# Optimization experiments

Measured on AMD Instinct MI355X. Metric: run time of the kernel, lower is better.

The kernel has to match this reference:

```python
import jax, jax.numpy as jnp
import numpy as np

NUM_HEADS = 8
NUM_GROUPS = 32
EPS = 1e-5


def setup_inputs() -> dict:
    key = jax.random.key(0)
    ks = jax.random.split(key, 3)
    B, C, T = 4, 512, 2048
    x = jax.random.normal(ks[0], (B, C, T), dtype=jnp.float32)
    gn_gamma = jnp.ones((C,), jnp.float32)
    gn_beta = jnp.zeros((C,), jnp.float32)
    w_qkv = jax.random.normal(ks[1], (3 * C, C), jnp.float32) * (1.0 / np.sqrt(C))
    b_qkv = jnp.zeros((3 * C,), jnp.float32)
    w_proj = jax.random.normal(ks[2], (C, C), jnp.float32) * (1.0 / np.sqrt(C))
    b_proj = jnp.zeros((C,), jnp.float32)
    return {"x": x, "gn_gamma": gn_gamma, "gn_beta": gn_beta,
            "w_qkv": w_qkv, "b_qkv": b_qkv, "w_proj": w_proj, "b_proj": b_proj}


def _group_norm(x, gamma, beta):
    # x: [B, C, T]
    B, C, T = x.shape
    xg = x.reshape(B, NUM_GROUPS, (C // NUM_GROUPS) * T)
    mean = xg.mean(axis=-1, keepdims=True)
    var = xg.var(axis=-1, keepdims=True)
    xn = ((xg - mean) * jax.lax.rsqrt(var + EPS)).reshape(B, C, T)
    return xn * gamma[None, :, None] + beta[None, :, None]


def reference(x, gn_gamma, gn_beta, w_qkv, b_qkv, w_proj, b_proj):
    B, C, T = x.shape
    H = NUM_HEADS
    dh = C // H  # attn_ch
    scale = 1.0 / np.sqrt(np.sqrt(dh))

    h = _group_norm(x, gn_gamma, gn_beta)
    # 1x1 conv1d == channel matmul: [B, 3C, T]
    qkv = jnp.einsum('oc,bct->bot', w_qkv, h) + b_qkv[None, :, None]
    # tokens-major: [B, T, H, 3*dh]
    qkv = qkv.transpose(0, 2, 1).reshape(B, T, H, 3 * dh)
    q, k, v = jnp.split(qkv, 3, axis=-1)  # each [B, T, H, dh]

    weight = jnp.einsum('bthc,bshc->bhts', q * scale, k * scale)
    weight = jax.nn.softmax(weight.astype(jnp.float32), axis=-1).astype(qkv.dtype)
    out = jnp.einsum('bhts,bshc->bthc', weight, v).reshape(B, T, C)

    out = out.transpose(0, 2, 1)  # [B, C, T]
    y = jnp.einsum('oc,bct->bot', w_proj, out) + b_proj[None, :, None]
    return x + y
```

## Files before the change

### kernel.cpp

```cpp
#include <hip/hip_runtime.h>
#include <hip/hip_bf16.h>
#include <math.h>
#include <stdint.h>

#define Bb 4
#define Cc 512
#define Tt 2048
#define Hh 8

typedef __attribute__((ext_vector_type(8))) short short8;
typedef __attribute__((ext_vector_type(4))) float f32x4;
typedef __attribute__((ext_vector_type(8))) unsigned short u16x8;

__device__ __forceinline__ unsigned short f2bf(float f) {
  __hip_bfloat16 h = __float2bfloat16(f);
  unsigned short u;
  __builtin_memcpy(&u, &h, 2);
  return u;
}
__device__ __forceinline__ float bf2f(unsigned short u) {
  union { uint32_t i; float f; } v;
  v.i = (uint32_t)u << 16;
  return v.f;
}

__device__ __forceinline__ void async16(const void* g, void* l) {
  __builtin_amdgcn_global_load_lds(
      (const __attribute__((address_space(1))) uint32_t*)g,
      (__attribute__((address_space(3))) uint32_t*)l, 16, 0, 0);
}

__global__ __launch_bounds__(256) void gn_part(const float* __restrict__ x,
                                               float* __restrict__ part) {
  const int blk = blockIdx.x;
  const size_t base = (size_t)blk * 4096;
  const int tid = threadIdx.x;
  float s = 0.f, ss = 0.f;
#pragma unroll
  for (int k = 0; k < 4; ++k) {
    const float4 v = *(const float4*)(x + base + (size_t)(k * 256 + tid) * 4);
    s += v.x + v.y + v.z + v.w;
    ss += v.x * v.x + v.y * v.y + v.z * v.z + v.w * v.w;
  }
#pragma unroll
  for (int off = 32; off >= 1; off >>= 1) {
    s += __shfl_down(s, off);
    ss += __shfl_down(ss, off);
  }
  __shared__ float rs[4], rss[4];
  const int wid = tid >> 6;
  if ((tid & 63) == 0) { rs[wid] = s; rss[wid] = ss; }
  __syncthreads();
  if (tid == 0) {
    part[blk * 2] = rs[0] + rs[1] + rs[2] + rs[3];
    part[blk * 2 + 1] = rss[0] + rss[1] + rss[2] + rss[3];
  }
}

__global__ __launch_bounds__(128) void gn_fin(const float* __restrict__ part,
                                              float* __restrict__ stats) {
  const int g = threadIdx.x;
  float s = 0.f, ss = 0.f;
#pragma unroll
  for (int c = 0; c < 8; ++c) {
    s += part[(g * 8 + c) * 2];
    ss += part[(g * 8 + c) * 2 + 1];
  }
  const float mean = s / 32768.f;
  const float var = ss / 32768.f - mean * mean;
  stats[g * 2] = mean;
  stats[g * 2 + 1] = rsqrtf(var + 1e-5f);
}

__global__ __launch_bounds__(256) void norm_trans(const float* __restrict__ x,
                                                  const float* __restrict__ stats,
                                                  const float* __restrict__ gamma,
                                                  const float* __restrict__ beta,
                                                  unsigned short* __restrict__ hT) {
  __shared__ unsigned short Tl[64][72];
  const int tid = threadIdx.x;
  const int b = blockIdx.z, c0 = blockIdx.y * 64, t0 = blockIdx.x * 64;
  const int cl = tid >> 2, j16 = (tid & 3) * 16;
  const int c = c0 + cl;
  const int grp = c >> 4;
  const float mean = stats[((size_t)b * 32 + grp) * 2];
  const float rstd = stats[((size_t)b * 32 + grp) * 2 + 1];
  const float ga = gamma[c] * rstd;
  const float be = beta[c] - mean * ga;
  const float* src = x + ((size_t)b * Cc + c) * Tt + t0 + j16;
#pragma unroll
  for (int q = 0; q < 4; ++q) {
    const float4 v = *(const float4*)(src + q * 4);
    Tl[j16 + q * 4 + 0][cl] = f2bf(v.x * ga + be);
    Tl[j16 + q * 4 + 1][cl] = f2bf(v.y * ga + be);
    Tl[j16 + q * 4 + 2][cl] = f2bf(v.z * ga + be);
    Tl[j16 + q * 4 + 3][cl] = f2bf(v.w * ga + be);
  }
  __syncthreads();
  const int tl = tid >> 2, i16 = (tid & 3) * 16;
  unsigned short* dst = hT + ((size_t)b * Tt + t0 + tl) * Cc + c0 + i16;
  *(u16x8*)dst = *(const u16x8*)&Tl[tl][i16];
  *(u16x8*)(dst + 8) = *(const u16x8*)&Tl[tl][i16 + 8];
}

__global__ __launch_bounds__(256) void cvt_bf16_2(const float* __restrict__ a,
                                                  unsigned short* __restrict__ oa, int n4a,
                                                  const float* __restrict__ bsrc,
                                                  unsigned short* __restrict__ ob, int n4b) {
  const int i = blockIdx.x * 256 + threadIdx.x;
  const float* in;
  unsigned short* out;
  int idx;
  if (i < n4a) {
    in = a; out = oa; idx = i;
  } else if (i < n4a + n4b) {
    in = bsrc; out = ob; idx = i - n4a;
  } else {
    return;
  }
  const float4 v = *(const float4*)(in + (size_t)idx * 4);
  ushort4 o;
  o.x = f2bf(v.x); o.y = f2bf(v.y); o.z = f2bf(v.z); o.w = f2bf(v.w);
  *(ushort4*)(out + (size_t)idx * 4) = o;
}

template <int MODE, int BM>
__global__ __launch_bounds__(256) void gemm_mfma(const unsigned short* __restrict__ A,
                                                 const unsigned short* __restrict__ Bt,
                                                 const float* __restrict__ bias,
                                                 const float* __restrict__ res,
                                                 unsigned short* __restrict__ outb,
                                                 float* __restrict__ outf,
                                                 unsigned short* __restrict__ qkt,
                                                 int M) {
  constexpr int NA = BM / 32;
  __shared__ unsigned short SMEM[(BM + 128) * 64];
  unsigned short* Al = SMEM;
  unsigned short* Bl = SMEM + BM * 64;
  const int tid = threadIdx.x;
  const int n0 = blockIdx.x * 128, m0 = blockIdx.y * BM;
  const size_t z = blockIdx.z;
  const int l = tid & 63, il = l & 15, g = l >> 4;
  const int w = tid >> 6;
  const int wm = (w >> 1) * (BM / 2), wn = (w & 1) * 64;

  const unsigned short* Bz = Bt + z * (size_t)Tt * Cc;
  const unsigned short* Ap = A + (size_t)(m0 + (tid >> 2)) * Cc + (tid & 3) * 8;
  const unsigned short* Bp = Bz + (size_t)(n0 + (tid >> 2)) * Cc + (tid & 3) * 8;
  char* ldsA = (char*)Al + w * 1024;
  char* ldsB = (char*)Bl + w * 1024;

  f32x4 acc[NA][4] = {};
  for (int k0 = 0; k0 < Cc; k0 += 64) {
#pragma unroll
    for (int ks = 0; ks < 2; ++ks) {
      const int ko = k0 + ks * 32;
      async16(Ap + ko, ldsA + ks * (BM * 64));
      if (BM == 128) async16(Ap + (size_t)64 * Cc + ko, ldsA + ks * (BM * 64) + 4096);
      async16(Bp + ko, ldsB + ks * (128 * 64));
      async16(Bp + (size_t)64 * Cc + ko, ldsB + ks * (128 * 64) + 4096);
    }
    __syncthreads();
    __builtin_amdgcn_s_setprio(1);
#pragma unroll
    for (int ks = 0; ks < 2; ++ks) {
      short8 af[NA], bf[4];
#pragma unroll
      for (int i = 0; i < NA; ++i)
        af[i] = *(const short8*)(Al + ks * (BM * 32) + (wm + i * 16 + il) * 32 + g * 8);
#pragma unroll
      for (int j = 0; j < 4; ++j)
        bf[j] = *(const short8*)(Bl + ks * (128 * 32) + (wn + j * 16 + il) * 32 + g * 8);
#pragma unroll
      for (int i = 0; i < NA; ++i)
#pragma unroll
        for (int j = 0; j < 4; ++j)
          acc[i][j] = __builtin_amdgcn_mfma_f32_16x16x32_bf16(af[i], bf[j], acc[i][j], 0, 0, 0);
    }
    __builtin_amdgcn_s_setprio(0);
    __syncthreads();
  }

  if (MODE == 1) {
#pragma unroll
    for (int i = 0; i < NA; ++i) {
#pragma unroll
      for (int r = 0; r < 4; ++r) {
        const int m = m0 + wm + i * 16 + 4 * g + r;
        const float bv = bias[m];
#pragma unroll
        for (int j = 0; j < 4; ++j) {
          const int n = n0 + wn + j * 16 + il;
          const size_t idx = (z * (size_t)M + m) * Tt + n;
          outf[idx] = acc[i][j][r] + bv + res[idx];
        }
      }
    }
  } else {
    const int r0 = m0 + wm;
    const int sec = (r0 % 192) >> 6;
    const int hh = r0 / 192;
    if (sec == 2) {
#pragma unroll
      for (int i = 0; i < 4; ++i) {
#pragma unroll
        for (int r = 0; r < 4; ++r) {
          const int m = r0 + i * 16 + 4 * g + r;
          const float bv = bias[m];
#pragma unroll
          for (int j = 0; j < 4; ++j) {
            const int n = n0 + wn + j * 16 + il;
            outb[(z * (size_t)M + m) * Tt + n] = f2bf(acc[i][j][r] + bv);
          }
        }
      }
    } else {
      unsigned short (*Sc)[32][72] = (unsigned short(*)[32][72])SMEM;
      const float qs = (sec == 0) ? 0.125f * 1.44269504f : 1.0f;
      const size_t obase = ((size_t)(z * (Hh * 2)) + hh * 2 + sec) * Tt;
#pragma unroll
      for (int hf = 0; hf < 2; ++hf) {
#pragma unroll
        for (int i = 0; i < 4; ++i) {
          const int mloc = i * 16 + 4 * g;
          const float b0 = bias[r0 + mloc + 0];
          const float b1 = bias[r0 + mloc + 1];
          const float b2 = bias[r0 + mloc + 2];
          const float b3 = bias[r0 + mloc + 3];
#pragma unroll
          for (int j2 = 0; j2 < 2; ++j2) {
            const int j = hf * 2 + j2;
            ushort4 pkk;
            pkk.x = f2bf((acc[i][j][0] + b0) * qs);
            pkk.y = f2bf((acc[i][j][1] + b1) * qs);
            pkk.z = f2bf((acc[i][j][2] + b2) * qs);
            pkk.w = f2bf((acc[i][j][3] + b3) * qs);
            *(ushort4*)&Sc[w][j2 * 16 + il][mloc] = pkk;
          }
        }
        asm volatile("s_waitcnt lgkmcnt(0)" ::: "memory");
#pragma unroll
        for (int it = 0; it < 4; ++it) {
          const int row = it * 8 + (l >> 3);
          const int mcol = (l & 7) * 8;
          const u16x8 vv = *(const u16x8*)&Sc[w][row][mcol];
          const int tg = n0 + wn + hf * 32 + row;
          *(u16x8*)(qkt + (obase + tg) * 64 + mcol) = vv;
        }
        asm volatile("s_waitcnt lgkmcnt(0)" ::: "memory");
      }
    }
  }
}

__global__ __launch_bounds__(256, 4) void attn_mfma5(const unsigned short* __restrict__ qkt,
                                                     const unsigned short* __restrict__ qkvc,
                                                     unsigned short* __restrict__ attnoT) {
  __shared__ unsigned short KVs[2][2][64 * 64];

  const int tid = threadIdx.x;
  const int w = tid >> 6, l = tid & 63, il = l & 15, g = l >> 4;

  const int bid = blockIdx.x;
  const int swz = (bid & 7) * 128 + (bid >> 3);
  const int bh = swz >> 5, qt = swz & 31;
  const int b = bh >> 3, h = bh & 7;
  const int q0 = qt * 64;

  const unsigned short* Qb = qkt + (size_t)(bh * 2) * Tt * 64;
  const char* Kb = (const char*)(Qb + (size_t)Tt * 64);
  const char* Vb = (const char*)(qkvc + ((size_t)b * (3 * Cc) + h * 192 + 128) * Tt);

  short8 qf[2];
  {
    const unsigned short* qp = Qb + (size_t)(q0 + w * 16 + il) * 64 + g * 8;
    qf[0] = *(const short8*)qp;
    qf[1] = *(const short8*)(qp + 32);
  }

  union { uint32_t u[4]; short8 v; } ones;
  ones.u[0] = ones.u[1] = ones.u[2] = ones.u[3] = 0x3F803F80u;

  float m_run = 0.f;
  f32x4 acco[4] = {};
  f32x4 acc_l = {};
  uint32_t frP[2][4];

  const int srow = w * 16 + (l >> 3);
  const int scol = ((l & 7) ^ (l >> 3)) << 4;

  auto stage = [&](int buf, int s0) {
    char* kd = (char*)&KVs[buf][0][0] + w * 2048;
    char* vd = (char*)&KVs[buf][1][0] + w * 2048;
    async16(Kb + (size_t)(s0 + srow) * 128 + scol, kd);
    async16(Kb + (size_t)(s0 + srow + 8) * 128 + scol, kd + 1024);
    async16(Vb + (size_t)srow * (Tt * 2) + (size_t)s0 * 2 + scol, vd);
    async16(Vb + (size_t)(srow + 8) * (Tt * 2) + (size_t)s0 * 2 + scol, vd + 1024);
  };

  f32x4 accs[4];
  auto qk_phase = [&](int buf) {
    const float nm = -m_run;
#pragma unroll
    for (int i = 0; i < 4; ++i) {
      accs[i][0] = nm; accs[i][1] = nm; accs[i][2] = nm; accs[i][3] = nm;
    }
    const unsigned short* Kc = &KVs[buf][0][0];
#pragma unroll
    for (int ks = 0; ks < 2; ++ks) {
#pragma unroll
      for (int i = 0; i < 4; ++i) {
        const short8 kf =
            *(const short8*)(Kc + (i * 16 + il) * 64 + ((((ks << 2) + g) ^ (il & 7)) << 3));
        accs[i] = __builtin_amdgcn_mfma_f32_16x16x32_bf16(kf, qf[ks], accs[i], 0, 0, 0);
      }
    }
  };

  auto pv_phase = [&](int buf) {
    const unsigned short* Vc = &KVs[buf][1][0];
#pragma unroll
    for (int ks = 0; ks < 2; ++ks) {
      union { uint32_t u[4]; short8 v; } fu;
      fu.u[0] = frP[ks][0]; fu.u[1] = frP[ks][1];
      fu.u[2] = frP[ks][2]; fu.u[3] = frP[ks][3];
#pragma unroll
      for (int j = 0; j < 4; ++j) {
        const short8 vf =
            *(const short8*)(Vc + (j * 16 + il) * 64 + ((((ks << 2) + g) ^ (il & 7)) << 3));
        acco[j] = __builtin_amdgcn_mfma_f32_16x16x32_bf16(fu.v, vf, acco[j], 0, 0, 0);
      }
      acc_l = __builtin_amdgcn_mfma_f32_16x16x32_bf16(fu.v, ones.v, acc_l, 0, 0, 0);
    }
  };

  auto softmax_pack = [&]() {
    float pmax = fmaxf(fmaxf(fmaxf(accs[0][0], accs[0][1]), accs[0][2]), accs[0][3]);
    pmax = fmaxf(pmax, fmaxf(fmaxf(accs[1][0], accs[1][1]), fmaxf(accs[1][2], accs[1][3])));
    pmax = fmaxf(pmax, fmaxf(fmaxf(accs[2][0], accs[2][1]), fmaxf(accs[2][2], accs[2][3])));
    pmax = fmaxf(pmax, fmaxf(fmaxf(accs[3][0], accs[3][1]), fmaxf(accs[3][2], accs[3][3])));

    uint32_t pk[4][2];
    if (!__all(pmax <= 8.0f)) {
      float mx = pmax;
#pragma unroll
      for (int off = 1; off < 64; off <<= 1) mx = fmaxf(mx, __shfl_xor(mx, off));
      const float alpha = __builtin_amdgcn_exp2f(-mx);
      m_run += mx;
#pragma unroll
      for (int j = 0; j < 4; ++j) acco[j] = acco[j] * alpha;
      acc_l = acc_l * alpha;
#pragma unroll
      for (int i = 0; i < 4; ++i) {
        const float p0 = __builtin_amdgcn_exp2f(accs[i][0] - mx);
        const float p1 = __builtin_amdgcn_exp2f(accs[i][1] - mx);
        const float p2 = __builtin_amdgcn_exp2f(accs[i][2] - mx);
        const float p3 = __builtin_amdgcn_exp2f(accs[i][3] - mx);
        asm("v_cvt_pk_bf16_f32 %0, %1, %2" : "=v"(pk[i][0]) : "v"(p0), "v"(p1));
        asm("v_cvt_pk_bf16_f32 %0, %1, %2" : "=v"(pk[i][1]) : "v"(p2), "v"(p3));
      }
    } else {
#pragma unroll
      for (int i = 0; i < 4; ++i) {
        const float p0 = __builtin_amdgcn_exp2f(accs[i][0]);
        const float p1 = __builtin_amdgcn_exp2f(accs[i][1]);
        const float p2 = __builtin_amdgcn_exp2f(accs[i][2]);
        const float p3 = __builtin_amdgcn_exp2f(accs[i][3]);
        asm("v_cvt_pk_bf16_f32 %0, %1, %2" : "=v"(pk[i][0]) : "v"(p0), "v"(p1));
        asm("v_cvt_pk_bf16_f32 %0, %1, %2" : "=v"(pk[i][1]) : "v"(p2), "v"(p3));
      }
    }
#pragma unroll
    for (int ks = 0; ks < 2; ++ks) {
#pragma unroll
      for (int hh = 0; hh < 2; ++hh) {
        uint32_t a = pk[2 * ks][hh], bq = pk[2 * ks + 1][hh];
        asm("v_permlane32_swap_b32 %0, %1" : "+v"(a), "+v"(bq));
        asm("v_permlane16_swap_b32 %0, %1" : "+v"(a), "+v"(bq));
        frP[ks][hh] = a;
        frP[ks][2 + hh] = bq;
      }
    }
  };

  stage(0, 0);
  __syncthreads();
  stage(1, 64);
  __builtin_amdgcn_s_setprio(1);
  qk_phase(0);
  __builtin_amdgcn_s_setprio(0);
  softmax_pack();

  const int NT = Tt / 64;
  for (int t = 1; t < NT; ++t) {
    const int cb = t & 1, pb = cb ^ 1;
    __syncthreads();
    __builtin_amdgcn_s_setprio(1);
    qk_phase(cb);
    pv_phase(pb);
    __builtin_amdgcn_s_setprio(0);
    __syncthreads();
    if (t + 1 < NT) stage(pb, (t + 1) * 64);
    softmax_pack();
  }
  __builtin_amdgcn_s_setprio(1);
  pv_phase(1);
  __builtin_amdgcn_s_setprio(0);

#pragma unroll
  for (int r = 0; r < 4; ++r) {
    const float li = 1.f / acc_l[r];
    const int tq = q0 + w * 16 + 4 * g + r;
    unsigned short* d0 = attnoT + ((size_t)b * Tt + tq) * Cc + h * 64 + il;
#pragma unroll
    for (int j = 0; j < 4; ++j) d0[j * 16] = f2bf(acco[j][r] * li);
  }
}

extern "C" void kernel_launch(void* const* d_in, const int* in_sizes, int n_in,
                              void* d_out, int out_size, void* d_ws, size_t ws_size,
                              hipStream_t stream) {
  const float* x = (const float*)d_in[0];
  const float* gamma = (const float*)d_in[1];
  const float* beta = (const float*)d_in[2];
  const float* w_qkv = (const float*)d_in[3];
  const float* b_qkv = (const float*)d_in[4];
  const float* w_proj = (const float*)d_in[5];
  const float* b_proj = (const float*)d_in[6];
  float* out = (float*)d_out;

  char* p = (char*)d_ws;
  float* stats = (float*)p;                  p += 256 * sizeof(float);
  float* part = (float*)p;                   p += 2048 * sizeof(float);
  unsigned short* hT = (unsigned short*)p;   p += (size_t)Bb * Tt * Cc * 2;
  unsigned short* wq = (unsigned short*)p;   p += (size_t)3 * Cc * Cc * 2;
  unsigned short* wp = (unsigned short*)p;   p += (size_t)Cc * Cc * 2;
  unsigned short* qkvc = (unsigned short*)p; p += (size_t)Bb * 3 * Cc * Tt * 2;
  unsigned short* qkt = (unsigned short*)p;  p += (size_t)Bb * Hh * 2 * Tt * 64 * 2;
  unsigned short* attnoT = (unsigned short*)p;

  const int n4q = 3 * Cc * Cc / 4, n4p = Cc * Cc / 4;

  gn_part<<<dim3(1024), 256, 0, stream>>>(x, part);
  gn_fin<<<dim3(1), 128, 0, stream>>>(part, stats);
  norm_trans<<<dim3(Tt / 64, Cc / 64, Bb), 256, 0, stream>>>(x, stats, gamma, beta, hT);
  cvt_bf16_2<<<dim3((n4q + n4p + 255) / 256), 256, 0, stream>>>(w_qkv, wq, n4q, w_proj, wp, n4p);
  gemm_mfma<0, 128><<<dim3(Tt / 128, (3 * Cc) / 128, Bb), 256, 0, stream>>>(
      wq, hT, b_qkv, nullptr, qkvc, nullptr, qkt, 3 * Cc);
  attn_mfma5<<<dim3(1024), 256, 0, stream>>>(qkt, qkvc, attnoT);
  gemm_mfma<1, 64><<<dim3(Tt / 128, Cc / 64, Bb), 256, 0, stream>>>(
      wp, attnoT, b_proj, x, nullptr, out, nullptr, Cc);
}
```

Measured before the change: 111.4 us.

## Triple-buffer K tiles in attention and fold GroupNorm finalize into norm kernel

```diff
diff --git a/kernel.cpp b/kernel.cpp
--- a/kernel.cpp
+++ b/kernel.cpp
@@ -57,23 +57,8 @@
   }
 }
 
-__global__ __launch_bounds__(128) void gn_fin(const float* __restrict__ part,
-                                              float* __restrict__ stats) {
-  const int g = threadIdx.x;
-  float s = 0.f, ss = 0.f;
-#pragma unroll
-  for (int c = 0; c < 8; ++c) {
-    s += part[(g * 8 + c) * 2];
-    ss += part[(g * 8 + c) * 2 + 1];
-  }
-  const float mean = s / 32768.f;
-  const float var = ss / 32768.f - mean * mean;
-  stats[g * 2] = mean;
-  stats[g * 2 + 1] = rsqrtf(var + 1e-5f);
-}
-
 __global__ __launch_bounds__(256) void norm_trans(const float* __restrict__ x,
-                                                  const float* __restrict__ stats,
+                                                  const float* __restrict__ part,
                                                   const float* __restrict__ gamma,
                                                   const float* __restrict__ beta,
                                                   unsigned short* __restrict__ hT) {
@@ -83,8 +68,14 @@
   const int cl = tid >> 2, j16 = (tid & 3) * 16;
   const int c = c0 + cl;
   const int grp = c >> 4;
-  const float mean = stats[((size_t)b * 32 + grp) * 2];
-  const float rstd = stats[((size_t)b * 32 + grp) * 2 + 1];
+  float s = 0.f, ss = 0.f;
+#pragma unroll
+  for (int i = 0; i < 8; ++i) {
+    s += part[(b * 256 + grp * 8 + i) * 2];
+    ss += part[(b * 256 + grp * 8 + i) * 2 + 1];
+  }
+  const float mean = s * (1.f / 32768.f);
+  const float rstd = rsqrtf(ss * (1.f / 32768.f) - mean * mean + 1e-5f);
   const float ga = gamma[c] * rstd;
   const float be = beta[c] - mean * ga;
   const float* src = x + ((size_t)b * Cc + c) * Tt + t0 + j16;
@@ -253,10 +244,11 @@
   }
 }
 
-__global__ __launch_bounds__(256, 4) void attn_mfma5(const unsigned short* __restrict__ qkt,
+__global__ __launch_bounds__(256, 4) void attn_mfma7(const unsigned short* __restrict__ qkt,
                                                      const unsigned short* __restrict__ qkvc,
                                                      unsigned short* __restrict__ attnoT) {
-  __shared__ unsigned short KVs[2][2][64 * 64];
+  __shared__ unsigned short Kbuf[3][64 * 64];
+  __shared__ unsigned short Vbuf[2][64 * 64];
 
   const int tid = threadIdx.x;
   const int w = tid >> 6, l = tid & 63, il = l & 15, g = l >> 4;
@@ -289,23 +281,24 @@
   const int srow = w * 16 + (l >> 3);
   const int scol = ((l & 7) ^ (l >> 3)) << 4;
 
-  auto stage = [&](int buf, int s0) {
-    char* kd = (char*)&KVs[buf][0][0] + w * 2048;
-    char* vd = (char*)&KVs[buf][1][0] + w * 2048;
+  auto stageK = [&](int buf, int s0) {
+    char* kd = (char*)&Kbuf[buf][0] + w * 2048;
     async16(Kb + (size_t)(s0 + srow) * 128 + scol, kd);
     async16(Kb + (size_t)(s0 + srow + 8) * 128 + scol, kd + 1024);
+  };
+  auto stageV = [&](int buf, int s0) {
+    char* vd = (char*)&Vbuf[buf][0] + w * 2048;
     async16(Vb + (size_t)srow * (Tt * 2) + (size_t)s0 * 2 + scol, vd);
     async16(Vb + (size_t)(srow + 8) * (Tt * 2) + (size_t)s0 * 2 + scol, vd + 1024);
   };
 
   f32x4 accs[4];
-  auto qk_phase = [&](int buf) {
+  auto qk_phase = [&](const unsigned short* Kc) {
     const float nm = -m_run;
 #pragma unroll
     for (int i = 0; i < 4; ++i) {
       accs[i][0] = nm; accs[i][1] = nm; accs[i][2] = nm; accs[i][3] = nm;
     }
-    const unsigned short* Kc = &KVs[buf][0][0];
 #pragma unroll
     for (int ks = 0; ks < 2; ++ks) {
 #pragma unroll
@@ -317,8 +310,7 @@
     }
   };
 
-  auto pv_phase = [&](int buf) {
-    const unsigned short* Vc = &KVs[buf][1][0];
+  auto pv_phase = [&](const unsigned short* Vc) {
 #pragma unroll
     for (int ks = 0; ks < 2; ++ks) {
       union { uint32_t u[4]; short8 v; } fu;
@@ -383,28 +375,34 @@
     }
   };
 
-  stage(0, 0);
-  __syncthreads();
-  stage(1, 64);
+  stageK(0, 0);   stageV(0, 0);
+  stageK(1, 64);  stageV(1, 64);
+  asm volatile("s_waitcnt vmcnt(4)\n\ts_barrier" ::: "memory");
+  stageK(2, 128);
   __builtin_amdgcn_s_setprio(1);
-  qk_phase(0);
+  qk_phase(&Kbuf[0][0]);
   __builtin_amdgcn_s_setprio(0);
   softmax_pack();
 
   const int NT = Tt / 64;
   for (int t = 1; t < NT; ++t) {
-    const int cb = t & 1, pb = cb ^ 1;
-    __syncthreads();
+    if (t == 1 || t == NT - 1) {
+      asm volatile("s_waitcnt vmcnt(2)\n\ts_barrier" ::: "memory");
+    } else {
+      asm volatile("s_waitcnt vmcnt(4)\n\ts_barrier" ::: "memory");
+    }
     __builtin_amdgcn_s_setprio(1);
-    qk_phase(cb);
-    pv_phase(pb);
+    qk_phase(&Kbuf[t % 3][0]);
+    pv_phase(&Vbuf[(t - 1) & 1][0]);
     __builtin_amdgcn_s_setprio(0);
-    __syncthreads();
-    if (t + 1 < NT) stage(pb, (t + 1) * 64);
+    asm volatile("s_barrier" ::: "memory");
+    if (t + 2 < NT) stageK((t + 2) % 3, (t + 2) * 64);
+    if (t + 1 < NT) stageV((t + 1) & 1, (t + 1) * 64);
     softmax_pack();
   }
+  asm volatile("s_waitcnt vmcnt(0)\n\ts_barrier" ::: "memory");
   __builtin_amdgcn_s_setprio(1);
-  pv_phase(1);
+  pv_phase(&Vbuf[(NT - 1) & 1][0]);
   __builtin_amdgcn_s_setprio(0);
 
 #pragma unroll
@@ -430,7 +428,6 @@
   float* out = (float*)d_out;
 
   char* p = (char*)d_ws;
-  float* stats = (float*)p;                  p += 256 * sizeof(float);
   float* part = (float*)p;                   p += 2048 * sizeof(float);
   unsigned short* hT = (unsigned short*)p;   p += (size_t)Bb * Tt * Cc * 2;
   unsigned short* wq = (unsigned short*)p;   p += (size_t)3 * Cc * Cc * 2;
@@ -442,12 +439,11 @@
   const int n4q = 3 * Cc * Cc / 4, n4p = Cc * Cc / 4;
 
   gn_part<<<dim3(1024), 256, 0, stream>>>(x, part);
-  gn_fin<<<dim3(1), 128, 0, stream>>>(part, stats);
-  norm_trans<<<dim3(Tt / 64, Cc / 64, Bb), 256, 0, stream>>>(x, stats, gamma, beta, hT);
+  norm_trans<<<dim3(Tt / 64, Cc / 64, Bb), 256, 0, stream>>>(x, part, gamma, beta, hT);
   cvt_bf16_2<<<dim3((n4q + n4p + 255) / 256), 256, 0, stream>>>(w_qkv, wq, n4q, w_proj, wp, n4p);
   gemm_mfma<0, 128><<<dim3(Tt / 128, (3 * Cc) / 128, Bb), 256, 0, stream>>>(
       wq, hT, b_qkv, nullptr, qkvc, nullptr, qkt, 3 * Cc);
-  attn_mfma5<<<dim3(1024), 256, 0, stream>>>(qkt, qkvc, attnoT);
+  attn_mfma7<<<dim3(1024), 256, 0, stream>>>(qkt, qkvc, attnoT);
   gemm_mfma<1, 64><<<dim3(Tt / 128, Cc / 64, Bb), 256, 0, stream>>>(
       wp, attnoT, b_proj, x, nullptr, out, nullptr, Cc);
 }
```

Measured after the change: 109.4 us. About the same (-1.8%).

## Double query rows per attention wave and fold group-norm finalize into normalize

Applied to the files above, without the earlier changes.

```diff
diff --git a/kernel.cpp b/kernel.cpp
--- a/kernel.cpp
+++ b/kernel.cpp
@@ -57,23 +57,8 @@
   }
 }
 
-__global__ __launch_bounds__(128) void gn_fin(const float* __restrict__ part,
-                                              float* __restrict__ stats) {
-  const int g = threadIdx.x;
-  float s = 0.f, ss = 0.f;
-#pragma unroll
-  for (int c = 0; c < 8; ++c) {
-    s += part[(g * 8 + c) * 2];
-    ss += part[(g * 8 + c) * 2 + 1];
-  }
-  const float mean = s / 32768.f;
-  const float var = ss / 32768.f - mean * mean;
-  stats[g * 2] = mean;
-  stats[g * 2 + 1] = rsqrtf(var + 1e-5f);
-}
-
 __global__ __launch_bounds__(256) void norm_trans(const float* __restrict__ x,
-                                                  const float* __restrict__ stats,
+                                                  const float* __restrict__ part,
                                                   const float* __restrict__ gamma,
                                                   const float* __restrict__ beta,
                                                   unsigned short* __restrict__ hT) {
@@ -83,8 +68,14 @@
   const int cl = tid >> 2, j16 = (tid & 3) * 16;
   const int c = c0 + cl;
   const int grp = c >> 4;
-  const float mean = stats[((size_t)b * 32 + grp) * 2];
-  const float rstd = stats[((size_t)b * 32 + grp) * 2 + 1];
+  float s = 0.f, ss = 0.f;
+#pragma unroll
+  for (int i = 0; i < 8; ++i) {
+    s += part[(b * 256 + grp * 8 + i) * 2];
+    ss += part[(b * 256 + grp * 8 + i) * 2 + 1];
+  }
+  const float mean = s * (1.f / 32768.f);
+  const float rstd = rsqrtf(ss * (1.f / 32768.f) - mean * mean + 1e-5f);
   const float ga = gamma[c] * rstd;
   const float be = beta[c] - mean * ga;
   const float* src = x + ((size_t)b * Cc + c) * Tt + t0 + j16;
@@ -253,7 +244,7 @@
   }
 }
 
-__global__ __launch_bounds__(256, 4) void attn_mfma5(const unsigned short* __restrict__ qkt,
+__global__ __launch_bounds__(256, 2) void attn_mfma9(const unsigned short* __restrict__ qkt,
                                                      const unsigned short* __restrict__ qkvc,
                                                      unsigned short* __restrict__ attnoT) {
   __shared__ unsigned short KVs[2][2][64 * 64];
@@ -262,29 +253,31 @@
   const int w = tid >> 6, l = tid & 63, il = l & 15, g = l >> 4;
 
   const int bid = blockIdx.x;
-  const int swz = (bid & 7) * 128 + (bid >> 3);
-  const int bh = swz >> 5, qt = swz & 31;
+  const int swz = (bid & 7) * 64 + (bid >> 3);
+  const int bh = swz >> 4, qt = swz & 15;
   const int b = bh >> 3, h = bh & 7;
-  const int q0 = qt * 64;
+  const int q0 = qt * 128;
 
   const unsigned short* Qb = qkt + (size_t)(bh * 2) * Tt * 64;
   const char* Kb = (const char*)(Qb + (size_t)Tt * 64);
   const char* Vb = (const char*)(qkvc + ((size_t)b * (3 * Cc) + h * 192 + 128) * Tt);
 
-  short8 qf[2];
+  short8 qf0[2], qf1[2];
   {
-    const unsigned short* qp = Qb + (size_t)(q0 + w * 16 + il) * 64 + g * 8;
-    qf[0] = *(const short8*)qp;
-    qf[1] = *(const short8*)(qp + 32);
+    const unsigned short* qp = Qb + (size_t)(q0 + w * 32 + il) * 64 + g * 8;
+    qf0[0] = *(const short8*)qp;
+    qf0[1] = *(const short8*)(qp + 32);
+    qf1[0] = *(const short8*)(qp + 16 * 64);
+    qf1[1] = *(const short8*)(qp + 16 * 64 + 32);
   }
 
   union { uint32_t u[4]; short8 v; } ones;
   ones.u[0] = ones.u[1] = ones.u[2] = ones.u[3] = 0x3F803F80u;
 
-  float m_run = 0.f;
-  f32x4 acco[4] = {};
-  f32x4 acc_l = {};
-  uint32_t frP[2][4];
+  float m_run0 = 0.f, m_run1 = 0.f;
+  f32x4 acco0[4] = {}, acco1[4] = {};
+  f32x4 acc_l0 = {}, acc_l1 = {};
+  uint32_t frP0[2][4], frP1[2][4];
 
   const int srow = w * 16 + (l >> 3);
   const int scol = ((l & 7) ^ (l >> 3)) << 4;
@@ -298,12 +291,13 @@
     async16(Vb + (size_t)(srow + 8) * (Tt * 2) + (size_t)s0 * 2 + scol, vd + 1024);
   };
 
-  f32x4 accs[4];
+  f32x4 accs0[4], accs1[4];
   auto qk_phase = [&](int buf) {
-    const float nm = -m_run;
+    const float nm0 = -m_run0, nm1 = -m_run1;
 #pragma unroll
     for (int i = 0; i < 4; ++i) {
-      accs[i][0] = nm; accs[i][1] = nm; accs[i][2] = nm; accs[i][3] = nm;
+      accs0[i][0] = nm0; accs0[i][1] = nm0; accs0[i][2] = nm0; accs0[i][3] = nm0;
+      accs1[i][0] = nm1; accs1[i][1] = nm1; accs1[i][2] = nm1; accs1[i][3] = nm1;
     }
     const unsigned short* Kc = &KVs[buf][0][0];
 #pragma unroll
@@ -312,7 +306,8 @@
       for (int i = 0; i < 4; ++i) {
         const short8 kf =
             *(const short8*)(Kc + (i * 16 + il) * 64 + ((((ks << 2) + g) ^ (il & 7)) << 3));
-        accs[i] = __builtin_amdgcn_mfma_f32_16x16x32_bf16(kf, qf[ks], accs[i], 0, 0, 0);
+        accs0[i] = __builtin_amdgcn_mfma_f32_16x16x32_bf16(kf, qf0[ks], accs0[i], 0, 0, 0);
+        accs1[i] = __builtin_amdgcn_mfma_f32_16x16x32_bf16(kf, qf1[ks], accs1[i], 0, 0, 0);
       }
     }
   };
@@ -321,20 +316,25 @@
     const unsigned short* Vc = &KVs[buf][1][0];
 #pragma unroll
     for (int ks = 0; ks < 2; ++ks) {
-      union { uint32_t u[4]; short8 v; } fu;
-      fu.u[0] = frP[ks][0]; fu.u[1] = frP[ks][1];
-      fu.u[2] = frP[ks][2]; fu.u[3] = frP[ks][3];
+      union { uint32_t u[4]; short8 v; } fu0, fu1;
+      fu0.u[0] = frP0[ks][0]; fu0.u[1] = frP0[ks][1];
+      fu0.u[2] = frP0[ks][2]; fu0.u[3] = frP0[ks][3];
+      fu1.u[0] = frP1[ks][0]; fu1.u[1] = frP1[ks][1];
+      fu1.u[2] = frP1[ks][2]; fu1.u[3] = frP1[ks][3];
 #pragma unroll
       for (int j = 0; j < 4; ++j) {
         const short8 vf =
             *(const short8*)(Vc + (j * 16 + il) * 64 + ((((ks << 2) + g) ^ (il & 7)) << 3));
-        acco[j] = __builtin_amdgcn_mfma_f32_16x16x32_bf16(fu.v, vf, acco[j], 0, 0, 0);
-      }
-      acc_l = __builtin_amdgcn_mfma_f32_16x16x32_bf16(fu.v, ones.v, acc_l, 0, 0, 0);
+        acco0[j] = __builtin_amdgcn_mfma_f32_16x16x32_bf16(fu0.v, vf, acco0[j], 0, 0, 0);
+        acco1[j] = __builtin_amdgcn_mfma_f32_16x16x32_bf16(fu1.v, vf, acco1[j], 0, 0, 0);
+      }
+      acc_l0 = __builtin_amdgcn_mfma_f32_16x16x32_bf16(fu0.v, ones.v, acc_l0, 0, 0, 0);
+      acc_l1 = __builtin_amdgcn_mfma_f32_16x16x32_bf16(fu1.v, ones.v, acc_l1, 0, 0, 0);
     }
   };
 
-  auto softmax_pack = [&]() {
+  auto softmax_one = [&](f32x4 (&accs)[4], f32x4 (&acco)[4], f32x4& acc_l,
+                         float& m_run, uint32_t (&frP)[2][4]) {
     float pmax = fmaxf(fmaxf(fmaxf(accs[0][0], accs[0][1]), accs[0][2]), accs[0][3]);
     pmax = fmaxf(pmax, fmaxf(fmaxf(accs[1][0], accs[1][1]), fmaxf(accs[1][2], accs[1][3])));
     pmax = fmaxf(pmax, fmaxf(fmaxf(accs[2][0], accs[2][1]), fmaxf(accs[2][2], accs[2][3])));
@@ -389,7 +389,8 @@
   __builtin_amdgcn_s_setprio(1);
   qk_phase(0);
   __builtin_amdgcn_s_setprio(0);
-  softmax_pack();
+  softmax_one(accs0, acco0, acc_l0, m_run0, frP0);
+  softmax_one(accs1, acco1, acc_l1, m_run1, frP1);
 
   const int NT = Tt / 64;
   for (int t = 1; t < NT; ++t) {
@@ -401,7 +402,8 @@
     __builtin_amdgcn_s_setprio(0);
     __syncthreads();
     if (t + 1 < NT) stage(pb, (t + 1) * 64);
-    softmax_pack();
+    softmax_one(accs0, acco0, acc_l0, m_run0, frP0);
+    softmax_one(accs1, acco1, acc_l1, m_run1, frP1);
   }
   __builtin_amdgcn_s_setprio(1);
   pv_phase(1);
@@ -409,11 +411,16 @@
 
 #pragma unroll
   for (int r = 0; r < 4; ++r) {
-    const float li = 1.f / acc_l[r];
-    const int tq = q0 + w * 16 + 4 * g + r;
+    const float li0 = 1.f / acc_l0[r];
+    const float li1 = 1.f / acc_l1[r];
+    const int tq = q0 + w * 32 + 4 * g + r;
     unsigned short* d0 = attnoT + ((size_t)b * Tt + tq) * Cc + h * 64 + il;
-#pragma unroll
-    for (int j = 0; j < 4; ++j) d0[j * 16] = f2bf(acco[j][r] * li);
+    unsigned short* d1 = attnoT + ((size_t)b * Tt + tq + 16) * Cc + h * 64 + il;
+#pragma unroll
+    for (int j = 0; j < 4; ++j) {
+      d0[j * 16] = f2bf(acco0[j][r] * li0);
+      d1[j * 16] = f2bf(acco1[j][r] * li1);
+    }
   }
 }
 
@@ -430,7 +437,6 @@
   float* out = (float*)d_out;
 
   char* p = (char*)d_ws;
-  float* stats = (float*)p;                  p += 256 * sizeof(float);
   float* part = (float*)p;                   p += 2048 * sizeof(float);
   unsigned short* hT = (unsigned short*)p;   p += (size_t)Bb * Tt * Cc * 2;
   unsigned short* wq = (unsigned short*)p;   p += (size_t)3 * Cc * Cc * 2;
@@ -442,12 +448,11 @@
   const int n4q = 3 * Cc * Cc / 4, n4p = Cc * Cc / 4;
 
   gn_part<<<dim3(1024), 256, 0, stream>>>(x, part);
-  gn_fin<<<dim3(1), 128, 0, stream>>>(part, stats);
-  norm_trans<<<dim3(Tt / 64, Cc / 64, Bb), 256, 0, stream>>>(x, stats, gamma, beta, hT);
+  norm_trans<<<dim3(Tt / 64, Cc / 64, Bb), 256, 0, stream>>>(x, part, gamma, beta, hT);
   cvt_bf16_2<<<dim3((n4q + n4p + 255) / 256), 256, 0, stream>>>(w_qkv, wq, n4q, w_proj, wp, n4p);
   gemm_mfma<0, 128><<<dim3(Tt / 128, (3 * Cc) / 128, Bb), 256, 0, stream>>>(
       wq, hT, b_qkv, nullptr, qkvc, nullptr, qkt, 3 * Cc);
-  attn_mfma5<<<dim3(1024), 256, 0, stream>>>(qkt, qkvc, attnoT);
+  attn_mfma9<<<dim3(512), 256, 0, stream>>>(qkt, qkvc, attnoT);
   gemm_mfma<1, 64><<<dim3(Tt / 128, Cc / 64, Bb), 256, 0, stream>>>(
       wp, attnoT, b_proj, x, nullptr, out, nullptr, Cc);
 }
```

Result: faster. 99.80 us (-10.4%).
